# Optimization experiments

Hardware: AMD Instinct MI355X
Metric: run time of the kernel (lower is better)

## Reference

```python
import jax, jax.numpy as jnp
import numpy as np

NC = 64      # num_channels per whitening group
T = 5        # Newton-Schulz iterations
EPS = 1e-5


def setup_inputs() -> dict:
    key = jax.random.key(0)
    x = jax.random.normal(key, (64, 256, 56, 56), dtype=jnp.float32)
    weight = jnp.ones((1, 256, 1, 1), dtype=jnp.float32)
    bias = jnp.zeros((1, 256, 1, 1), dtype=jnp.float32)
    return {"x": x, "weight": weight, "bias": bias}


def _iternorm_whiten(X):
    B, C, H, W = X.shape
    g = C // NC
    # (g, nc, m) with m = B*H*W, matching X.transpose(0,1).view(g, nc, -1)
    xv = jnp.transpose(X, (1, 0, 2, 3)).reshape(g, NC, -1)
    m = xv.shape[-1]
    mean = xv.mean(-1, keepdims=True)          # (g, nc, 1)
    xc = xv - mean
    I = jnp.eye(NC, dtype=X.dtype)
    # Sigma = eps*I + xc @ xc^T / m   (baddbmm with beta=eps, alpha=1/m)
    Sigma = EPS * I + jnp.einsum('gdm,gem->gde', xc, xc) / m
    rTr = 1.0 / jnp.trace(Sigma, axis1=1, axis2=2)[:, None, None]  # (g,1,1)
    Sn = Sigma * rTr
    P = jnp.broadcast_to(I, (g, NC, NC))
    for _ in range(T):
        P3 = P @ P @ P
        P = 1.5 * P - 0.5 * (P3 @ Sn)
    wm = P * jnp.sqrt(rTr)                     # whitening matrix per group
    xn = wm @ xc                               # (g, nc, m)
    Xn = jnp.transpose(xn.reshape(C, B, H, W), (1, 0, 2, 3))
    return Xn


def reference(x, weight, bias):
    return _iternorm_whiten(x) * weight + bias
```

## Files before the change

kernel.cpp:

```cpp
#include <hip/hip_runtime.h>
#include <hip/hip_bf16.h>


#define B_    64
#define C_    256
#define HW_   3136
#define G_    4
#define NC_   64
#define M_    (B_*HW_)
#define EPS_  1e-5f
#define TIT_  5

#define NGB_  1024
#define PBLK_ 256

typedef __attribute__((ext_vector_type(8))) short  s16x8;
typedef __attribute__((ext_vector_type(4))) float  f32x4;

#define MFMA_(A,Bv,Cc) Cc = __builtin_amdgcn_mfma_f32_16x16x32_bf16(A, Bv, Cc, 0, 0, 0)

__device__ __forceinline__ unsigned short f2bf(float f){
  union{ float f; unsigned int u; } c; c.f = f;
  unsigned int u = c.u;
  u = u + 0x7FFFu + ((u >> 16) & 1u);
  return (unsigned short)(u >> 16);
}
__device__ __forceinline__ float bf2f(unsigned short h){
  union{ unsigned int u; float f; } c; c.u = ((unsigned int)h) << 16;
  return c.f;
}
__device__ __forceinline__ int swz(int off, int row){
  return off ^ ((row & 7) << 4) ^ (((row >> 3) & 3) << 5);
}
__device__ __forceinline__ s16x8 ld_frag(const unsigned short* base, int row, int kbyte){
  return *(const s16x8*)((const char*)base + swz(row*128 + kbyte, row));
}
__device__ __forceinline__ void st_h(unsigned short* base, int row, int col, unsigned short v){
  *(unsigned short*)((char*)base + swz(row*128 + col*2, row)) = v;
}
__device__ __forceinline__ unsigned short ld_h(const unsigned short* base, int row, int col){
  return *(const unsigned short*)((const char*)base + swz(row*128 + col*2, row));
}

template<bool ATOMIC>
__global__ __launch_bounds__(256) void k_gram(const float* __restrict__ x,
                                              float* __restrict__ S1,
                                              float* __restrict__ S2,
                                              float* __restrict__ partS2,
                                              float* __restrict__ partS1){
  __shared__ __align__(16) unsigned short tile[3][64*64];
  const int tid  = threadIdx.x;
  const int lane = tid & 63, wave = tid >> 6;
  const int bx   = blockIdx.x;
  const int g = bx >> 8, sub = bx & 255, b = sub >> 2, quad = sub & 3;
  const int ck0 = (quad*49) >> 2, ck1 = ((quad+1)*49) >> 2;
  const int nck = ck1 - ck0;
  const float* xg = x + ((size_t)b*C_ + (size_t)g*NC_) * HW_;
  const int chb = (tid >> 4) * 4;
  const int posoff = (tid & 15) * 4;
  const int wrow = (wave >> 1) * 32, wcol = (wave & 1) * 32;
  float s1a[4] = {0.f,0.f,0.f,0.f};
  f32x4 acc[2][2] = {};
  float v[4][4];

  auto load_c = [&](int ck){
    #pragma unroll
    for(int q = 0; q < 4; ++q){
      const float4 t = *(const float4*)(xg + (size_t)(chb+q)*HW_ + ck*64 + posoff);
      v[q][0]=t.x; v[q][1]=t.y; v[q][2]=t.z; v[q][3]=t.w;
    }
  };
  auto write_c = [&](unsigned short* tl){
    #pragma unroll
    for(int q = 0; q < 4; ++q){
      s1a[q] += v[q][0]+v[q][1]+v[q][2]+v[q][3];
      const int ch = chb + q;
      const unsigned long long pk =
            (unsigned long long)f2bf(v[q][0])
          | ((unsigned long long)f2bf(v[q][1]) << 16)
          | ((unsigned long long)f2bf(v[q][2]) << 32)
          | ((unsigned long long)f2bf(v[q][3]) << 48);
      *(unsigned long long*)((char*)tl + swz(ch*128 + posoff*2, ch)) = pk;
    }
  };
  auto comp = [&](const unsigned short* tl){
    #pragma unroll
    for(int ks = 0; ks < 2; ++ks){
      const int kbyte = ks*64 + (lane >> 4) * 16;
      s16x8 a0 = ld_frag(tl, wrow +      (lane & 15), kbyte);
      s16x8 a1 = ld_frag(tl, wrow + 16 + (lane & 15), kbyte);
      s16x8 b0 = ld_frag(tl, wcol +      (lane & 15), kbyte);
      s16x8 b1 = ld_frag(tl, wcol + 16 + (lane & 15), kbyte);
      MFMA_(a0, b0, acc[0][0]);
      MFMA_(a0, b1, acc[0][1]);
      MFMA_(a1, b0, acc[1][0]);
      MFMA_(a1, b1, acc[1][1]);
    }
  };

  load_c(ck0);
  write_c(tile[0]);
  if(nck > 1) load_c(ck0 + 1);
  __syncthreads();
  for(int i = 0; i < nck; ++i){
    if(i + 1 < nck) write_c(tile[(i+1)%3]);
    if(i + 2 < nck) load_c(ck0 + i + 2);
    comp(tile[i%3]);
    __syncthreads();
  }

  if(ATOMIC){
    float* S2g = S2 + g * (NC_*NC_);
    #pragma unroll
    for(int i = 0; i < 2; ++i)
    #pragma unroll
    for(int j = 0; j < 2; ++j)
    #pragma unroll
    for(int r = 0; r < 4; ++r){
      const int d = wrow + 16*i + (lane >> 4)*4 + r;
      const int e = wcol + 16*j + (lane & 15);
      atomicAdd(&S2g[d*NC_ + e], acc[i][j][r]);
    }
  }else{
    float* p2 = partS2 + (size_t)bx*4096 + tid*16;
    #pragma unroll
    for(int i = 0; i < 2; ++i)
    #pragma unroll
    for(int j = 0; j < 2; ++j)
      *(f32x4*)(p2 + (i*2+j)*4) = acc[i][j];
  }
  #pragma unroll
  for(int q = 0; q < 4; ++q){
    float s = s1a[q];
    #pragma unroll
    for(int m2 = 1; m2 < 16; m2 <<= 1) s += __shfl_xor(s, m2, 64);
    if((lane & 15) == 0){
      if(ATOMIC) atomicAdd(&S1[g*NC_ + chb + q], s);
      else       partS1[(size_t)bx*64 + chb + q] = s;
    }
  }
}

__global__ __launch_bounds__(256) void k_reduce(const float* __restrict__ partS2,
                                                const float* __restrict__ partS1,
                                                float* __restrict__ S1,
                                                float* __restrict__ S2){
  const int bid = blockIdx.x, tid = threadIdx.x;
  const int sub = tid & 3;
  if(bid < 256){
    const int flat = (bid*256 + tid) >> 2;
    const int g = flat >> 12, t = flat & 4095;
    const float* p = partS2 + ((size_t)(g*PBLK_ + sub*64))*4096 + t;
    float s = 0.f;
    for(int jb = 0; jb < 64; ++jb) s += p[(size_t)jb*4096];
    s += __shfl_xor(s, 1, 64);
    s += __shfl_xor(s, 2, 64);
    if(sub == 0){
      const int tt = t >> 4, q = (t >> 2) & 3, r = t & 3;
      const int wave = tt >> 6, lane = tt & 63;
      const int d = (wave >> 1)*32 + ((q >> 1) << 4) + ((lane >> 4) << 2) + r;
      const int e = (wave &  1)*32 + ((q &  1) << 4) + (lane & 15);
      S2[g*4096 + d*64 + e] = s;
    }
  }else{
    const int g = bid - 256, ch = tid >> 2;
    const float* p = partS1 + ((size_t)(g*PBLK_ + sub*64))*64 + ch;
    float s = 0.f;
    for(int jb = 0; jb < 64; ++jb) s += p[(size_t)jb*64];
    s += __shfl_xor(s, 1, 64);
    s += __shfl_xor(s, 2, 64);
    if(sub == 0) S1[g*NC_ + ch] = s;
  }
}

__device__ __forceinline__ void mm_core(f32x4 acc[2][2],
    const unsigned short* Ah, const unsigned short* Al,
    const unsigned short* Bh, const unsigned short* Bl,
    int lane, int wrow, int wcol){
  #pragma unroll
  for(int ks = 0; ks < 2; ++ks){
    const int kbyte = ks*64 + (lane >> 4) * 16;
    s16x8 ah0 = ld_frag(Ah, wrow +      (lane & 15), kbyte);
    s16x8 ah1 = ld_frag(Ah, wrow + 16 + (lane & 15), kbyte);
    s16x8 al0 = ld_frag(Al, wrow +      (lane & 15), kbyte);
    s16x8 al1 = ld_frag(Al, wrow + 16 + (lane & 15), kbyte);
    s16x8 bh0 = ld_frag(Bh, wcol +      (lane & 15), kbyte);
    s16x8 bh1 = ld_frag(Bh, wcol + 16 + (lane & 15), kbyte);
    s16x8 bl0 = ld_frag(Bl, wcol +      (lane & 15), kbyte);
    s16x8 bl1 = ld_frag(Bl, wcol + 16 + (lane & 15), kbyte);
    MFMA_(ah0, bh0, acc[0][0]); MFMA_(ah0, bl0, acc[0][0]); MFMA_(al0, bh0, acc[0][0]);
    MFMA_(ah0, bh1, acc[0][1]); MFMA_(ah0, bl1, acc[0][1]); MFMA_(al0, bh1, acc[0][1]);
    MFMA_(ah1, bh0, acc[1][0]); MFMA_(ah1, bl0, acc[1][0]); MFMA_(al1, bh0, acc[1][0]);
    MFMA_(ah1, bh1, acc[1][1]); MFMA_(ah1, bl1, acc[1][1]); MFMA_(al1, bh1, acc[1][1]);
  }
}

__device__ __forceinline__ void mm64(unsigned short* dH, unsigned short* dL,
    const unsigned short* Ah, const unsigned short* Al,
    const unsigned short* Bh, const unsigned short* Bl,
    int lane, int wrow, int wcol){
  f32x4 acc[2][2] = {};
  mm_core(acc, Ah, Al, Bh, Bl, lane, wrow, wcol);
  #pragma unroll
  for(int i = 0; i < 2; ++i)
  #pragma unroll
  for(int j = 0; j < 2; ++j)
  #pragma unroll
  for(int r = 0; r < 4; ++r){
    const int d = wrow + 16*i + (lane >> 4)*4 + r;
    const int e = wcol + 16*j + (lane & 15);
    const float v = acc[i][j][r];
    const unsigned short h = f2bf(v);
    st_h(dH, d, e, h);
    st_h(dL, d, e, f2bf(v - bf2f(h)));
  }
}

__device__ __forceinline__ void ns_update(unsigned short* dH, unsigned short* dL,
    const unsigned short* Zh, const unsigned short* Zl,
    const unsigned short* Snh, const unsigned short* Snl,
    const unsigned short* pH, const unsigned short* pL,
    int lane, int wrow, int wcol){
  f32x4 acc[2][2] = {};
  mm_core(acc, Zh, Zl, Snh, Snl, lane, wrow, wcol);
  #pragma unroll
  for(int i = 0; i < 2; ++i)
  #pragma unroll
  for(int j = 0; j < 2; ++j)
  #pragma unroll
  for(int r = 0; r < 4; ++r){
    const int d = wrow + 16*i + (lane >> 4)*4 + r;
    const int e = wcol + 16*j + (lane & 15);
    const float pv = bf2f(ld_h(pH, d, e)) + bf2f(ld_h(pL, d, e));
    const float v = 1.5f*pv - 0.5f*acc[i][j][r];
    const unsigned short h = f2bf(v);
    st_h(dH, d, e, h);
    st_h(dL, d, e, f2bf(v - bf2f(h)));
  }
}

__global__ __launch_bounds__(256) void k_ns(const float* __restrict__ S1,
                                            const float* __restrict__ S2,
                                            const float* __restrict__ weight,
                                            const float* __restrict__ bias,
                                            float* __restrict__ wm,
                                            float* __restrict__ beta){
  __shared__ __align__(16) unsigned short smem[8*4096];
  unsigned short* Snh = smem;
  unsigned short* Snl = smem + 1*4096;
  unsigned short* Xh  = smem + 2*4096;
  unsigned short* Xl  = smem + 3*4096;
  unsigned short* Yh  = smem + 4*4096;
  unsigned short* Yl  = smem + 5*4096;
  unsigned short* Zh  = smem + 6*4096;
  unsigned short* Zl  = smem + 7*4096;
  const int g = blockIdx.x, tid = threadIdx.x;
  const int lane = tid & 63, wave = tid >> 6;
  const float* S1g = S1 + g*NC_;
  const float* S2g = S2 + g*NC_*NC_;
  const float invm = 1.0f / (float)M_;

  float term;
  {
    const float mui = S1g[lane] * invm;
    term = S2g[lane*NC_ + lane]*invm - mui*mui + EPS_;
    #pragma unroll
    for(int m2 = 1; m2 < 64; m2 <<= 1) term += __shfl_xor(term, m2, 64);
  }
  const float rTr  = 1.0f / term;
  const float srtr = sqrtf(rTr);

  {
    const int d  = tid >> 2;
    const int e0 = (tid & 3) * 16;
    const float mud = S1g[d] * invm;
    for(int k = 0; k < 16; ++k){
      const int e = e0 + k;
      const float mue = S1g[e] * invm;
      const float s = (S2g[d*NC_ + e]*invm - mud*mue + ((d==e)?EPS_:0.f)) * rTr;
      const unsigned short h = f2bf(s);
      st_h(Snh, d, e, h);
      st_h(Snl, d, e, f2bf(s - bf2f(h)));
      st_h(Xh,  d, e, (d==e)?(unsigned short)0x3F80:(unsigned short)0);
      st_h(Xl,  d, e, (unsigned short)0);
    }
  }
  __syncthreads();

  unsigned short *pH = Xh, *pL = Xl, *qH = Yh, *qL = Yl;
  const int wrow = (wave >> 1)*32, wcol = (wave & 1)*32;
  for(int it = 0; it < TIT_; ++it){
    mm64(qH, qL, pH, pL, pH, pL, lane, wrow, wcol);
    __syncthreads();
    mm64(Zh, Zl, qH, qL, pH, pL, lane, wrow, wcol);
    __syncthreads();
    ns_update(qH, qL, Zh, Zl, Snh, Snl, pH, pL, lane, wrow, wcol);
    __syncthreads();
    unsigned short* t;
    t = pH; pH = qH; qH = t;
    t = pL; pL = qL; qL = t;
  }

  float* wmg = wm + g*NC_*NC_;
  const int d  = tid >> 2;
  const int e0 = (tid & 3) * 16;
  float rs = 0.f;
  for(int k = 0; k < 16; ++k){
    const int e = e0 + k;
    const float wv = (bf2f(ld_h(pH, d, e)) + bf2f(ld_h(pL, d, e))) * srtr;
    wmg[d*NC_ + e] = wv;
    rs += wv * (S1g[e] * invm);
  }
  rs += __shfl_xor(rs, 1, 64);
  rs += __shfl_xor(rs, 2, 64);
  if((tid & 3) == 0)
    beta[g*NC_ + d] = bias[g*NC_ + d] - weight[g*NC_ + d] * rs;
}

__global__ __launch_bounds__(256) void k_apply(const float* __restrict__ x,
                                               const float* __restrict__ wm,
                                               const float* __restrict__ beta,
                                               const float* __restrict__ weight,
                                               float* __restrict__ out){
  __shared__ __align__(16) unsigned short tileT[3][64*64];
  const int tid  = threadIdx.x;
  const int lane = tid & 63, wave = tid >> 6;
  const int bx   = blockIdx.x;
  const int g = bx >> 9, sub = bx & 511, b = sub >> 3, oct = sub & 7;
  const int ck0 = (oct*49) >> 3, ck1 = ((oct+1)*49) >> 3;
  const int nck = ck1 - ck0;
  const float* xg = x   + ((size_t)b*C_ + (size_t)g*NC_) * HW_;
  float*       og = out + ((size_t)b*C_ + (size_t)g*NC_) * HW_;
  const int chb = (tid >> 4) * 4;
  const int posoff = (tid & 15) * 4;

  const float* wmg = wm + g*NC_*NC_;
  const int arow = wave*16 + (lane & 15);
  s16x8 ah[2], al[2];
  #pragma unroll
  for(int ks = 0; ks < 2; ++ks){
    const int kc = ks*32 + (lane >> 4)*8;
    const float* p = wmg + arow*NC_ + kc;
    #pragma unroll
    for(int j = 0; j < 8; ++j){
      const float w = p[j];
      const unsigned short h = f2bf(w);
      ah[ks][j] = (short)h;
      al[ks][j] = (short)f2bf(w - bf2f(h));
    }
  }
  const int cl = wave*16 + (lane & 15);
  const float wt = weight[g*NC_ + cl];
  const float bt = beta  [g*NC_ + cl];

  float v[4][4];
  auto load_c = [&](int ck){
    #pragma unroll
    for(int q = 0; q < 4; ++q){
      const float4 t = *(const float4*)(xg + (size_t)(chb+q)*HW_ + ck*64 + posoff);
      v[q][0]=t.x; v[q][1]=t.y; v[q][2]=t.z; v[q][3]=t.w;
    }
  };
  auto write_c = [&](unsigned short* tl){
    #pragma unroll
    for(int r = 0; r < 4; ++r){
      const int p = posoff + r;
      const unsigned long long pk =
            (unsigned long long)f2bf(v[0][r])
          | ((unsigned long long)f2bf(v[1][r]) << 16)
          | ((unsigned long long)f2bf(v[2][r]) << 32)
          | ((unsigned long long)f2bf(v[3][r]) << 48);
      *(unsigned long long*)((char*)tl + p*128 + ((chb*2) ^ ((p & 7) << 4))) = pk;
    }
  };
  auto comp = [&](const unsigned short* tl, int p0){
    #pragma unroll
    for(int tn = 0; tn < 4; ++tn){
      f32x4 acc = {0.f,0.f,0.f,0.f};
      const int pos = tn*16 + (lane & 15);
      #pragma unroll
      for(int ks = 0; ks < 2; ++ks){
        const int cb = (ks*64 + (lane >> 4)*16) ^ ((pos & 7) << 4);
        const s16x8 afr = *(const s16x8*)((const char*)tl + pos*128 + cb);
        MFMA_(afr, ah[ks], acc);
        MFMA_(afr, al[ks], acc);
      }
      const int pr = p0 + tn*16 + ((lane >> 4) << 2);
      f32x4 o;
      o[0] = acc[0]*wt + bt;
      o[1] = acc[1]*wt + bt;
      o[2] = acc[2]*wt + bt;
      o[3] = acc[3]*wt + bt;
      __builtin_nontemporal_store(o, (f32x4*)(og + (size_t)cl*HW_ + pr));
    }
  };

  load_c(ck0);
  write_c(tileT[0]);
  if(nck > 1) load_c(ck0 + 1);
  __syncthreads();
  for(int i = 0; i < nck; ++i){
    if(i + 1 < nck) write_c(tileT[(i+1)%3]);
    if(i + 2 < nck) load_c(ck0 + i + 2);
    comp(tileT[i%3], (ck0 + i)*64);
    __syncthreads();
  }
}

extern "C" void kernel_launch(void* const* d_in, const int* in_sizes, int n_in,
                              void* d_out, int out_size, void* d_ws, size_t ws_size,
                              hipStream_t stream){
  (void)in_sizes; (void)n_in; (void)out_size;
  const float* x  = (const float*)d_in[0];
  const float* w  = (const float*)d_in[1];
  const float* bs = (const float*)d_in[2];
  float* out  = (float*)d_out;
  float* S1   = (float*)d_ws;
  float* S2   = S1 + 256;
  float* beta = S2 + G_*NC_*NC_;
  float* wm   = beta + 256;
  float* p2   = wm + G_*NC_*NC_;
  float* p1   = p2 + (size_t)NGB_*4096;
  const size_t need = ((size_t)(256 + G_*4096 + 256 + G_*4096)
                       + (size_t)NGB_*4096 + (size_t)NGB_*64) * sizeof(float);
  if(ws_size >= need){
    k_gram<false><<<NGB_, 256, 0, stream>>>(x, S1, S2, p2, p1);
    k_reduce<<<260, 256, 0, stream>>>(p2, p1, S1, S2);
  }else{
    hipError_t _e = hipMemsetAsync(d_ws, 0, (256 + G_*NC_*NC_)*sizeof(float), stream);
    (void)_e;
    k_gram<true><<<NGB_, 256, 0, stream>>>(x, S1, S2, p2, p1);
  }
  k_ns   <<<G_,   256, 0, stream>>>(S1, S2, w, bs, wm, beta);
  k_apply<<<2048, 256, 0, stream>>>(x, wm, beta, w, out);
}
```

Before: 150.4 us.

## Cache bf16 copy of x in gram pass and read it in apply

The gram kernel now also writes its bf16-packed x tile to a workspace buffer, and the apply kernel reads that half-size copy instead of the fp32 input. The aim is to cut the second pass's read traffic. The cost is an extra write of the bf16 copy (about 100MB) plus a larger workspace requirement, so the net effect on DRAM traffic is roughly neutral unless the copy hits in cache. LDS buffering also drops from three tiles to two in both kernels.

```diff
diff --git a/kernel.cpp b/kernel.cpp
--- a/kernel.cpp
+++ b/kernel.cpp
@@ -42,20 +42,23 @@
   return *(const unsigned short*)((const char*)base + swz(row*128 + col*2, row));
 }
 
-template<bool ATOMIC>
+template<bool ATOMIC, bool XCACHE>
 __global__ __launch_bounds__(256) void k_gram(const float* __restrict__ x,
                                               float* __restrict__ S1,
                                               float* __restrict__ S2,
                                               float* __restrict__ partS2,
-                                              float* __restrict__ partS1){
-  __shared__ __align__(16) unsigned short tile[3][64*64];
+                                              float* __restrict__ partS1,
+                                              unsigned short* __restrict__ xb){
+  __shared__ __align__(16) unsigned short tile[2][64*64];
   const int tid  = threadIdx.x;
   const int lane = tid & 63, wave = tid >> 6;
   const int bx   = blockIdx.x;
   const int g = bx >> 8, sub = bx & 255, b = sub >> 2, quad = sub & 3;
   const int ck0 = (quad*49) >> 2, ck1 = ((quad+1)*49) >> 2;
   const int nck = ck1 - ck0;
-  const float* xg = x + ((size_t)b*C_ + (size_t)g*NC_) * HW_;
+  const size_t base = ((size_t)b*C_ + (size_t)g*NC_) * HW_;
+  const float* xg = x + base;
+  unsigned short* xbg = XCACHE ? (xb + base) : nullptr;
   const int chb = (tid >> 4) * 4;
   const int posoff = (tid & 15) * 4;
   const int wrow = (wave >> 1) * 32, wcol = (wave & 1) * 32;
@@ -70,7 +73,7 @@
       v[q][0]=t.x; v[q][1]=t.y; v[q][2]=t.z; v[q][3]=t.w;
     }
   };
-  auto write_c = [&](unsigned short* tl){
+  auto write_c = [&](unsigned short* tl, int ck){
     #pragma unroll
     for(int q = 0; q < 4; ++q){
       s1a[q] += v[q][0]+v[q][1]+v[q][2]+v[q][3];
@@ -81,6 +84,8 @@
           | ((unsigned long long)f2bf(v[q][2]) << 32)
           | ((unsigned long long)f2bf(v[q][3]) << 48);
       *(unsigned long long*)((char*)tl + swz(ch*128 + posoff*2, ch)) = pk;
+      if(XCACHE)
+        *(unsigned long long*)(xbg + (size_t)ch*HW_ + ck*64 + posoff) = pk;
     }
   };
   auto comp = [&](const unsigned short* tl){
@@ -99,13 +104,13 @@
   };
 
   load_c(ck0);
-  write_c(tile[0]);
+  write_c(tile[0], ck0);
   if(nck > 1) load_c(ck0 + 1);
   __syncthreads();
   for(int i = 0; i < nck; ++i){
-    if(i + 1 < nck) write_c(tile[(i+1)%3]);
+    if(i + 1 < nck) write_c(tile[(i+1)&1], ck0 + i + 1);
     if(i + 2 < nck) load_c(ck0 + i + 2);
-    comp(tile[i%3]);
+    comp(tile[i&1]);
     __syncthreads();
   }
 
@@ -317,20 +322,24 @@
     beta[g*NC_ + d] = bias[g*NC_ + d] - weight[g*NC_ + d] * rs;
 }
 
+template<bool XCACHE>
 __global__ __launch_bounds__(256) void k_apply(const float* __restrict__ x,
+                                               const unsigned short* __restrict__ xb,
                                                const float* __restrict__ wm,
                                                const float* __restrict__ beta,
                                                const float* __restrict__ weight,
                                                float* __restrict__ out){
-  __shared__ __align__(16) unsigned short tileT[3][64*64];
+  __shared__ __align__(16) unsigned short tileT[2][64*64];
   const int tid  = threadIdx.x;
   const int lane = tid & 63, wave = tid >> 6;
   const int bx   = blockIdx.x;
   const int g = bx >> 9, sub = bx & 511, b = sub >> 3, oct = sub & 7;
   const int ck0 = (oct*49) >> 3, ck1 = ((oct+1)*49) >> 3;
   const int nck = ck1 - ck0;
-  const float* xg = x   + ((size_t)b*C_ + (size_t)g*NC_) * HW_;
-  float*       og = out + ((size_t)b*C_ + (size_t)g*NC_) * HW_;
+  const size_t base = ((size_t)b*C_ + (size_t)g*NC_) * HW_;
+  const float*          xg  = x  + base;
+  const unsigned short* xg16 = XCACHE ? (xb + base) : nullptr;
+  float*                og  = out + base;
   const int chb = (tid >> 4) * 4;
   const int posoff = (tid & 15) * 4;
 
@@ -354,23 +363,41 @@
   const float bt = beta  [g*NC_ + cl];
 
   float v[4][4];
+  unsigned long long pkv[4];
   auto load_c = [&](int ck){
     #pragma unroll
     for(int q = 0; q < 4; ++q){
-      const float4 t = *(const float4*)(xg + (size_t)(chb+q)*HW_ + ck*64 + posoff);
-      v[q][0]=t.x; v[q][1]=t.y; v[q][2]=t.z; v[q][3]=t.w;
+      if(XCACHE){
+        pkv[q] = *(const unsigned long long*)(xg16 + (size_t)(chb+q)*HW_ + ck*64 + posoff);
+      }else{
+        const float4 t = *(const float4*)(xg + (size_t)(chb+q)*HW_ + ck*64 + posoff);
+        v[q][0]=t.x; v[q][1]=t.y; v[q][2]=t.z; v[q][3]=t.w;
+      }
     }
   };
   auto write_c = [&](unsigned short* tl){
-    #pragma unroll
-    for(int r = 0; r < 4; ++r){
-      const int p = posoff + r;
-      const unsigned long long pk =
-            (unsigned long long)f2bf(v[0][r])
-          | ((unsigned long long)f2bf(v[1][r]) << 16)
-          | ((unsigned long long)f2bf(v[2][r]) << 32)
-          | ((unsigned long long)f2bf(v[3][r]) << 48);
-      *(unsigned long long*)((char*)tl + p*128 + ((chb*2) ^ ((p & 7) << 4))) = pk;
+    if(XCACHE){
+      #pragma unroll
+      for(int r = 0; r < 4; ++r){
+        const int p = posoff + r;
+        const unsigned long long pk =
+              ((pkv[0] >> (16*r)) & 0xFFFFull)
+            | (((pkv[1] >> (16*r)) & 0xFFFFull) << 16)
+            | (((pkv[2] >> (16*r)) & 0xFFFFull) << 32)
+            | (((pkv[3] >> (16*r)) & 0xFFFFull) << 48);
+        *(unsigned long long*)((char*)tl + p*128 + ((chb*2) ^ ((p & 7) << 4))) = pk;
+      }
+    }else{
+      #pragma unroll
+      for(int r = 0; r < 4; ++r){
+        const int p = posoff + r;
+        const unsigned long long pk =
+              (unsigned long long)f2bf(v[0][r])
+            | ((unsigned long long)f2bf(v[1][r]) << 16)
+            | ((unsigned long long)f2bf(v[2][r]) << 32)
+            | ((unsigned long long)f2bf(v[3][r]) << 48);
+        *(unsigned long long*)((char*)tl + p*128 + ((chb*2) ^ ((p & 7) << 4))) = pk;
+      }
     }
   };
   auto comp = [&](const unsigned short* tl, int p0){
@@ -400,9 +427,9 @@
   if(nck > 1) load_c(ck0 + 1);
   __syncthreads();
   for(int i = 0; i < nck; ++i){
-    if(i + 1 < nck) write_c(tileT[(i+1)%3]);
+    if(i + 1 < nck) write_c(tileT[(i+1)&1]);
     if(i + 2 < nck) load_c(ck0 + i + 2);
-    comp(tileT[i%3], (ck0 + i)*64);
+    comp(tileT[i&1], (ck0 + i)*64);
     __syncthreads();
   }
 }
@@ -421,16 +448,25 @@
   float* wm   = beta + 256;
   float* p2   = wm + G_*NC_*NC_;
   float* p1   = p2 + (size_t)NGB_*4096;
-  const size_t need = ((size_t)(256 + G_*4096 + 256 + G_*4096)
-                       + (size_t)NGB_*4096 + (size_t)NGB_*64) * sizeof(float);
-  if(ws_size >= need){
-    k_gram<false><<<NGB_, 256, 0, stream>>>(x, S1, S2, p2, p1);
+  unsigned short* xb = (unsigned short*)(p1 + (size_t)NGB_*64);
+  const size_t need_nox = ((size_t)(256 + G_*4096 + 256 + G_*4096)
+                           + (size_t)NGB_*4096 + (size_t)NGB_*64) * sizeof(float);
+  const size_t need_x   = need_nox + (size_t)B_*C_*HW_*sizeof(unsigned short);
+  if(ws_size >= need_x){
+    k_gram<false,true><<<NGB_, 256, 0, stream>>>(x, S1, S2, p2, p1, xb);
     k_reduce<<<260, 256, 0, stream>>>(p2, p1, S1, S2);
+    k_ns   <<<G_,   256, 0, stream>>>(S1, S2, w, bs, wm, beta);
+    k_apply<true><<<2048, 256, 0, stream>>>(x, xb, wm, beta, w, out);
+  }else if(ws_size >= need_nox){
+    k_gram<false,false><<<NGB_, 256, 0, stream>>>(x, S1, S2, p2, p1, nullptr);
+    k_reduce<<<260, 256, 0, stream>>>(p2, p1, S1, S2);
+    k_ns   <<<G_,   256, 0, stream>>>(S1, S2, w, bs, wm, beta);
+    k_apply<false><<<2048, 256, 0, stream>>>(x, nullptr, wm, beta, w, out);
   }else{
     hipError_t _e = hipMemsetAsync(d_ws, 0, (256 + G_*NC_*NC_)*sizeof(float), stream);
     (void)_e;
-    k_gram<true><<<NGB_, 256, 0, stream>>>(x, S1, S2, p2, p1);
-  }
-  k_ns   <<<G_,   256, 0, stream>>>(S1, S2, w, bs, wm, beta);
-  k_apply<<<2048, 256, 0, stream>>>(x, wm, beta, w, out);
-}
+    k_gram<true,false><<<NGB_, 256, 0, stream>>>(x, S1, S2, p2, p1, nullptr);
+    k_ns   <<<G_,   256, 0, stream>>>(S1, S2, w, bs, wm, beta);
+    k_apply<false><<<2048, 256, 0, stream>>>(x, nullptr, wm, beta, w, out);
+  }
+}
```

After: 156.8 us. 1.04x slower.
